# Kernel tuning notes

Measured on AMD Instinct MI355X. Metric: run time of the kernel, lower is better.

## Reference

```python
import jax, jax.numpy as jnp
import numpy as np

N_NODES = 50000
D_FEAT = 128
N_EDGES = 500000


def setup_inputs() -> dict:
    key = jax.random.key(0)
    ks = jax.random.split(key, 9)
    scale1 = 1.0 / np.sqrt(2 * D_FEAT)
    scale2 = 1.0 / np.sqrt(512)
    scale3 = 1.0 / np.sqrt(256)
    return {
        "node_features": jax.random.normal(ks[0], (N_NODES, D_FEAT), dtype=jnp.float32),
        "edge_label_index": jax.random.randint(ks[1], (2, N_EDGES), 0, N_NODES, dtype=jnp.int64),
        "W1": jax.random.normal(ks[2], (512, 2 * D_FEAT), dtype=jnp.float32) * scale1,
        "b1": jax.random.normal(ks[3], (512,), dtype=jnp.float32) * scale1,
        "W2": jax.random.normal(ks[4], (256, 512), dtype=jnp.float32) * scale2,
        "b2": jax.random.normal(ks[5], (256,), dtype=jnp.float32) * scale2,
        "W3": jax.random.normal(ks[6], (1, 256), dtype=jnp.float32) * scale3,
        "b3": jax.random.normal(ks[7], (1,), dtype=jnp.float32) * scale3,
    }


def reference(node_features, edge_label_index, W1, b1, W2, b2, W3, b3):
    row = edge_label_index[0]
    col = edge_label_index[1]
    # [E, 2*d] gather + concat
    x = jnp.concatenate([node_features[row], node_features[col]], axis=-1)
    x = jax.nn.relu(x @ W1.T + b1)          # [E, 512]
    x = jax.nn.relu(x @ W2.T + b2)          # [E, 256]
    intermediate_x = x
    logits = x @ W3.T + b3                  # [E, 1]
    return (logits.reshape(-1), intermediate_x)
```

## Files before the change

kernel.cpp:

```cpp
#include <hip/hip_runtime.h>
#include <stdint.h>

#define E_TOT 500000
#define EB 64
#define NBLK ((E_TOT + EB - 1) / EB)
#define SWZ(e) (((e) & 7) << 4)
#define HOFF 32768

using u32x4  = __attribute__((ext_vector_type(4))) unsigned int;
using f32x4  = __attribute__((ext_vector_type(4))) float;
using short8 = __attribute__((ext_vector_type(8))) short;

__device__ __forceinline__ uint32_t f2bf(float x) {
    uint32_t u = __builtin_bit_cast(uint32_t, x);
    return (u + 0x7fffu + ((u >> 16) & 1u)) >> 16;
}
__device__ __forceinline__ uint32_t pk2(float a, float b) {
    return f2bf(a) | (f2bf(b) << 16);
}

__global__ void prep_weights(const float* __restrict__ W1, const float* __restrict__ W2,
                             unsigned short* __restrict__ w1b, unsigned short* __restrict__ w2b) {
    int t = blockIdx.x * 256 + threadIdx.x;
    int i = t * 4;
    if (i < 131072) {
        float4 f = *reinterpret_cast<const float4*>(W1 + i);
        uint2 u;
        u.x = pk2(f.x, f.y); u.y = pk2(f.z, f.w);
        *reinterpret_cast<uint2*>(w1b + i) = u;
    } else {
        int j = i - 131072;
        float4 f = *reinterpret_cast<const float4*>(W2 + j);
        uint2 u;
        u.x = pk2(f.x, f.y); u.y = pk2(f.z, f.w);
        *reinterpret_cast<uint2*>(w2b + j) = u;
    }
}

#define CHUNK(ABASE, MTSTR, LDSOFF, ACC, CUR, NXT, C, LAST)                                  \
  {                                                                                          \
    if (!(LAST)) {                                                                           \
      _Pragma("unroll") for (int kkl = 0; kkl < 2; ++kkl)                                    \
        _Pragma("unroll") for (int mt = 0; mt < 4; ++mt)                                     \
          NXT[kkl][mt] = *reinterpret_cast<const short8*>(                                   \
              (ABASE) + mt * (MTSTR) + (((C) + 1) * 2 + kkl) * 64);                          \
    }                                                                                        \
    _Pragma("unroll") for (int kkl = 0; kkl < 2; ++kkl) {                                    \
      const int kk = (C) * 2 + kkl;                                                          \
      short8 bfr[4];                                                                         \
      _Pragma("unroll") for (int nt = 0; nt < 4; ++nt) {                                     \
        const int boff = ((kk & 1) ? (bx0[nt] ^ 64) : bx0[nt]) + (LDSOFF) + (kk >> 1) * 128; \
        bfr[nt] = *reinterpret_cast<const short8*>(smem + boff);                             \
      }                                                                                      \
      _Pragma("unroll") for (int nt = 0; nt < 4; ++nt)                                       \
        _Pragma("unroll") for (int mt = 0; mt < 4; ++mt)                                     \
          ACC[mt][nt] = __builtin_amdgcn_mfma_f32_16x16x32_bf16(                             \
              CUR[kkl][mt], bfr[nt], ACC[mt][nt], 0, 0, 0);                                  \
    }                                                                                        \
  }

#define PHASE(ABASE, MTSTR, LDSOFF, ACC)                                                     \
  {                                                                                          \
    _Pragma("unroll") for (int kkl = 0; kkl < 2; ++kkl)                                      \
      _Pragma("unroll") for (int mt = 0; mt < 4; ++mt)                                       \
        Aa[kkl][mt] = *reinterpret_cast<const short8*>((ABASE) + mt * (MTSTR) + kkl * 64);   \
    CHUNK(ABASE, MTSTR, LDSOFF, ACC, Aa, Ab, 0, 0)                                           \
    CHUNK(ABASE, MTSTR, LDSOFF, ACC, Ab, Aa, 1, 0)                                           \
    CHUNK(ABASE, MTSTR, LDSOFF, ACC, Aa, Ab, 2, 0)                                           \
    CHUNK(ABASE, MTSTR, LDSOFF, ACC, Ab, Aa, 3, 1)                                           \
  }

template<bool PREPPED>
__global__ __launch_bounds__(256, 2) void fused_mlp(
    const float* __restrict__ nf,
    const int* __restrict__ eidx,
    const char* __restrict__ w1p,
    const char* __restrict__ w2p,
    const float* __restrict__ b1,
    const float* __restrict__ b2,
    const float* __restrict__ w3,
    const float* __restrict__ b3,
    float* __restrict__ out)
{
    __shared__ __align__(16) char smem[65536];
    __shared__ float logit_part[4][EB];

    const int tid  = threadIdx.x;
    const int lane = tid & 63;
    const int wid  = tid >> 6;
    const int hi   = lane >> 4;
    const int lo   = lane & 15;
    const long long e0 = (long long)blockIdx.x * EB;

    {
        int e    = tid >> 2;
        int side = (tid >> 1) & 1;
        int half = tid & 1;
        long long eg = e0 + e;
        int idx = 0;
        if (eg < E_TOT) idx = eidx[(size_t)side * E_TOT + (size_t)eg];
        const float4* src = reinterpret_cast<const float4*>(nf + (size_t)idx * 128 + half * 64);
        char* dstrow = smem + e * 512;
        const int ob = side * 256 + half * 128;
#pragma unroll
        for (int c = 0; c < 8; ++c) {
            float4 f0 = src[2 * c];
            float4 f1 = src[2 * c + 1];
            u32x4 u;
            u[0] = pk2(f0.x, f0.y); u[1] = pk2(f0.z, f0.w);
            u[2] = pk2(f1.x, f1.y); u[3] = pk2(f1.z, f1.w);
            *reinterpret_cast<u32x4*>(dstrow + ((ob + c * 16) ^ SWZ(e))) = u;
        }
    }

    int bx0[4];
#pragma unroll
    for (int nt = 0; nt < 4; ++nt) {
        int e   = nt * 16 + lo;
        int low = (hi * 16) ^ ((e & 3) << 4);
        int s6  = (e >> 2) & 1;
        bx0[nt] = e * 512 + low + 64 * s6;
    }

    __syncthreads();

    f32x4 acc2[4][4];
#pragma unroll
    for (int mt = 0; mt < 4; ++mt)
#pragma unroll
        for (int nt = 0; nt < 4; ++nt)
            acc2[mt][nt] = f32x4{0.f, 0.f, 0.f, 0.f};

    short8 Aa[2][4], Ab[2][4];

#pragma unroll
    for (int h = 0; h < 2; ++h) {
        f32x4 acc1[4][4];
#pragma unroll
        for (int mt = 0; mt < 4; ++mt)
#pragma unroll
            for (int nt = 0; nt < 4; ++nt)
                acc1[mt][nt] = f32x4{0.f, 0.f, 0.f, 0.f};

        if constexpr (PREPPED) {
            const char* a1b = w1p + (size_t)(h * 256 + wid * 64 + lo) * 512 + hi * 16;
            PHASE(a1b, (16 * 512), 0, acc1)
        } else {
            const float* W1f = reinterpret_cast<const float*>(w1p);
#pragma unroll
            for (int kk = 0; kk < 8; ++kk) {
                short8 a[4], b[4];
#pragma unroll
                for (int mt = 0; mt < 4; ++mt) {
                    const int row = h * 256 + wid * 64 + mt * 16 + lo;
                    const float* p = W1f + (size_t)row * 256 + kk * 32 + hi * 8;
                    float4 f0 = *reinterpret_cast<const float4*>(p);
                    float4 f1 = *reinterpret_cast<const float4*>(p + 4);
                    u32x4 u;
                    u[0] = pk2(f0.x, f0.y); u[1] = pk2(f0.z, f0.w);
                    u[2] = pk2(f1.x, f1.y); u[3] = pk2(f1.z, f1.w);
                    a[mt] = __builtin_bit_cast(short8, u);
                }
#pragma unroll
                for (int nt = 0; nt < 4; ++nt) {
                    const int boff = ((kk & 1) ? (bx0[nt] ^ 64) : bx0[nt]) + (kk >> 1) * 128;
                    b[nt] = *reinterpret_cast<const short8*>(smem + boff);
                }
#pragma unroll
                for (int nt = 0; nt < 4; ++nt)
#pragma unroll
                    for (int mt = 0; mt < 4; ++mt)
                        acc1[mt][nt] = __builtin_amdgcn_mfma_f32_16x16x32_bf16(a[mt], b[nt], acc1[mt][nt], 0, 0, 0);
            }
        }

#pragma unroll
        for (int mt = 0; mt < 4; ++mt) {
            const float4 bias = *reinterpret_cast<const float4*>(b1 + h * 256 + wid * 64 + mt * 16 + hi * 4);
            const int ob = wid * 128 + mt * 32 + hi * 8;
#pragma unroll
            for (int nt = 0; nt < 4; ++nt) {
                int e = nt * 16 + lo;
                f32x4 v = acc1[mt][nt];
                float r0 = fmaxf(v[0] + bias.x, 0.f);
                float r1 = fmaxf(v[1] + bias.y, 0.f);
                float r2 = fmaxf(v[2] + bias.z, 0.f);
                float r3 = fmaxf(v[3] + bias.w, 0.f);
                uint2 u;
                u.x = pk2(r0, r1); u.y = pk2(r2, r3);
                *reinterpret_cast<uint2*>(smem + HOFF + e * 512 + (ob ^ SWZ(e))) = u;
            }
        }
        __syncthreads();

        if constexpr (PREPPED) {
            const char* a2b = w2p + (size_t)(wid * 64 + lo) * 1024 + h * 512 + hi * 16;
            PHASE(a2b, (16 * 1024), HOFF, acc2)
        } else {
            const float* W2f = reinterpret_cast<const float*>(w2p);
#pragma unroll
            for (int kk = 0; kk < 8; ++kk) {
                short8 a[4], b[4];
#pragma unroll
                for (int mt = 0; mt < 4; ++mt) {
                    const int row = wid * 64 + mt * 16 + lo;
                    const float* p = W2f + (size_t)row * 512 + h * 256 + kk * 32 + hi * 8;
                    float4 f0 = *reinterpret_cast<const float4*>(p);
                    float4 f1 = *reinterpret_cast<const float4*>(p + 4);
                    u32x4 u;
                    u[0] = pk2(f0.x, f0.y); u[1] = pk2(f0.z, f0.w);
                    u[2] = pk2(f1.x, f1.y); u[3] = pk2(f1.z, f1.w);
                    a[mt] = __builtin_bit_cast(short8, u);
                }
#pragma unroll
                for (int nt = 0; nt < 4; ++nt) {
                    const int boff = ((kk & 1) ? (bx0[nt] ^ 64) : bx0[nt]) + HOFF + (kk >> 1) * 128;
                    b[nt] = *reinterpret_cast<const short8*>(smem + boff);
                }
#pragma unroll
                for (int nt = 0; nt < 4; ++nt)
#pragma unroll
                    for (int mt = 0; mt < 4; ++mt)
                        acc2[mt][nt] = __builtin_amdgcn_mfma_f32_16x16x32_bf16(a[mt], b[nt], acc2[mt][nt], 0, 0, 0);
            }
        }
        if (h == 0) __syncthreads();
    }

    {
        float* inter = out + E_TOT;
        float pls[4] = {0.f, 0.f, 0.f, 0.f};
#pragma unroll
        for (int mt = 0; mt < 4; ++mt) {
            const int m = wid * 64 + mt * 16 + hi * 4;
            const float4 bias = *reinterpret_cast<const float4*>(b2 + m);
            const float4 wv   = *reinterpret_cast<const float4*>(w3 + m);
#pragma unroll
            for (int nt = 0; nt < 4; ++nt) {
                long long eg = e0 + nt * 16 + lo;
                f32x4 v = acc2[mt][nt];
                float4 hh;
                hh.x = fmaxf(v[0] + bias.x, 0.f);
                hh.y = fmaxf(v[1] + bias.y, 0.f);
                hh.z = fmaxf(v[2] + bias.z, 0.f);
                hh.w = fmaxf(v[3] + bias.w, 0.f);
                if (eg < E_TOT)
                    *reinterpret_cast<float4*>(inter + (size_t)eg * 256 + m) = hh;
                pls[nt] += hh.x * wv.x + hh.y * wv.y + hh.z * wv.z + hh.w * wv.w;
            }
        }
#pragma unroll
        for (int nt = 0; nt < 4; ++nt) {
            float p = pls[nt];
            p += __shfl_xor(p, 16);
            p += __shfl_xor(p, 32);
            if (hi == 0) logit_part[wid][nt * 16 + lo] = p;
        }
    }
    __syncthreads();
    if (tid < EB) {
        long long eg = e0 + tid;
        if (eg < E_TOT) {
            float s = b3[0];
#pragma unroll
            for (int w = 0; w < 4; ++w) s += logit_part[w][tid];
            out[eg] = s;
        }
    }
}

extern "C" void kernel_launch(void* const* d_in, const int* in_sizes, int n_in,
                              void* d_out, int out_size, void* d_ws, size_t ws_size,
                              hipStream_t stream) {
    const float* nf   = (const float*)d_in[0];
    const int*   eidx = (const int*)d_in[1];
    const float* W1   = (const float*)d_in[2];
    const float* b1   = (const float*)d_in[3];
    const float* W2   = (const float*)d_in[4];
    const float* b2   = (const float*)d_in[5];
    const float* W3   = (const float*)d_in[6];
    const float* b3   = (const float*)d_in[7];
    float* out = (float*)d_out;

    const size_t need = (size_t)(512 * 256 + 256 * 512) * 2;
    if (ws_size >= need) {
        unsigned short* w1b = (unsigned short*)d_ws;
        unsigned short* w2b = w1b + 512 * 256;
        prep_weights<<<256, 256, 0, stream>>>(W1, W2, w1b, w2b);
        fused_mlp<true><<<NBLK, 256, 0, stream>>>(nf, eidx, (const char*)w1b, (const char*)w2b,
                                                  b1, b2, W3, b3, out);
    } else {
        fused_mlp<false><<<NBLK, 256, 0, stream>>>(nf, eidx, (const char*)W1, (const char*)W2,
                                                   b1, b2, W3, b3, out);
    }
}
```

Measured before the change: 587.4 us.

## Split layer-1 GEMM into half-width chunks and double-buffer A/B fragment loads

Layer 1 is now computed in two 32-row chunks per wave, so only 8 accumulator tiles are live instead of 16. This lowers register pressure next to the persistent layer-2 accumulators. The phase macro is rewritten to double-buffer both the global weight fragments and the LDS activation fragments one k-step ahead, where before only weights were prefetched two k-steps ahead. The cost is that each layer-1 chunk re-reads the LDS B fragments, doubling those reads, and the prefetch distance for global loads is shorter.

```diff
diff --git a/kernel.cpp b/kernel.cpp
--- a/kernel.cpp
+++ b/kernel.cpp
@@ -37,37 +37,31 @@
     }
 }
 
-#define CHUNK(ABASE, MTSTR, LDSOFF, ACC, CUR, NXT, C, LAST)                                  \
+#define PHASEPP(ABASE, MTSTR, NMT, LDSOFF, ACC)                                              \
   {                                                                                          \
-    if (!(LAST)) {                                                                           \
-      _Pragma("unroll") for (int kkl = 0; kkl < 2; ++kkl)                                    \
-        _Pragma("unroll") for (int mt = 0; mt < 4; ++mt)                                     \
-          NXT[kkl][mt] = *reinterpret_cast<const short8*>(                                   \
-              (ABASE) + mt * (MTSTR) + (((C) + 1) * 2 + kkl) * 64);                          \
-    }                                                                                        \
-    _Pragma("unroll") for (int kkl = 0; kkl < 2; ++kkl) {                                    \
-      const int kk = (C) * 2 + kkl;                                                          \
-      short8 bfr[4];                                                                         \
-      _Pragma("unroll") for (int nt = 0; nt < 4; ++nt) {                                     \
-        const int boff = ((kk & 1) ? (bx0[nt] ^ 64) : bx0[nt]) + (LDSOFF) + (kk >> 1) * 128; \
-        bfr[nt] = *reinterpret_cast<const short8*>(smem + boff);                             \
+    short8 Af[2][4];                                                                         \
+    short8 Bf[2][4];                                                                         \
+    _Pragma("unroll") for (int mt = 0; mt < (NMT); ++mt)                                     \
+      Af[0][mt] = *reinterpret_cast<const short8*>((ABASE) + mt * (MTSTR));                  \
+    _Pragma("unroll") for (int nt = 0; nt < 4; ++nt)                                         \
+      Bf[0][nt] = *reinterpret_cast<const short8*>(smem + bx0[nt] + (LDSOFF));               \
+    _Pragma("unroll") for (int kk = 0; kk < 8; ++kk) {                                       \
+      const int cur = kk & 1, nxt = cur ^ 1;                                                 \
+      if (kk < 7) {                                                                          \
+        _Pragma("unroll") for (int mt = 0; mt < (NMT); ++mt)                                 \
+          Af[nxt][mt] = *reinterpret_cast<const short8*>(                                    \
+              (ABASE) + mt * (MTSTR) + (kk + 1) * 64);                                       \
+        _Pragma("unroll") for (int nt = 0; nt < 4; ++nt) {                                   \
+          const int boff = (((kk + 1) & 1) ? (bx0[nt] ^ 64) : bx0[nt])                       \
+                           + (LDSOFF) + ((kk + 1) >> 1) * 128;                               \
+          Bf[nxt][nt] = *reinterpret_cast<const short8*>(smem + boff);                       \
+        }                                                                                    \
       }                                                                                      \
       _Pragma("unroll") for (int nt = 0; nt < 4; ++nt)                                       \
-        _Pragma("unroll") for (int mt = 0; mt < 4; ++mt)                                     \
+        _Pragma("unroll") for (int mt = 0; mt < (NMT); ++mt)                                 \
           ACC[mt][nt] = __builtin_amdgcn_mfma_f32_16x16x32_bf16(                             \
-              CUR[kkl][mt], bfr[nt], ACC[mt][nt], 0, 0, 0);                                  \
+              Af[cur][mt], Bf[cur][nt], ACC[mt][nt], 0, 0, 0);                               \
     }                                                                                        \
-  }
-
-#define PHASE(ABASE, MTSTR, LDSOFF, ACC)                                                     \
-  {                                                                                          \
-    _Pragma("unroll") for (int kkl = 0; kkl < 2; ++kkl)                                      \
-      _Pragma("unroll") for (int mt = 0; mt < 4; ++mt)                                       \
-        Aa[kkl][mt] = *reinterpret_cast<const short8*>((ABASE) + mt * (MTSTR) + kkl * 64);   \
-    CHUNK(ABASE, MTSTR, LDSOFF, ACC, Aa, Ab, 0, 0)                                           \
-    CHUNK(ABASE, MTSTR, LDSOFF, ACC, Ab, Aa, 1, 0)                                           \
-    CHUNK(ABASE, MTSTR, LDSOFF, ACC, Aa, Ab, 2, 0)                                           \
-    CHUNK(ABASE, MTSTR, LDSOFF, ACC, Ab, Aa, 3, 1)                                           \
   }
 
 template<bool PREPPED>
@@ -131,71 +125,73 @@
         for (int nt = 0; nt < 4; ++nt)
             acc2[mt][nt] = f32x4{0.f, 0.f, 0.f, 0.f};
 
-    short8 Aa[2][4], Ab[2][4];
-
 #pragma unroll
     for (int h = 0; h < 2; ++h) {
-        f32x4 acc1[4][4];
-#pragma unroll
-        for (int mt = 0; mt < 4; ++mt)
-#pragma unroll
-            for (int nt = 0; nt < 4; ++nt)
-                acc1[mt][nt] = f32x4{0.f, 0.f, 0.f, 0.f};
-
-        if constexpr (PREPPED) {
-            const char* a1b = w1p + (size_t)(h * 256 + wid * 64 + lo) * 512 + hi * 16;
-            PHASE(a1b, (16 * 512), 0, acc1)
-        } else {
-            const float* W1f = reinterpret_cast<const float*>(w1p);
-#pragma unroll
-            for (int kk = 0; kk < 8; ++kk) {
-                short8 a[4], b[4];
-#pragma unroll
-                for (int mt = 0; mt < 4; ++mt) {
-                    const int row = h * 256 + wid * 64 + mt * 16 + lo;
-                    const float* p = W1f + (size_t)row * 256 + kk * 32 + hi * 8;
-                    float4 f0 = *reinterpret_cast<const float4*>(p);
-                    float4 f1 = *reinterpret_cast<const float4*>(p + 4);
-                    u32x4 u;
-                    u[0] = pk2(f0.x, f0.y); u[1] = pk2(f0.z, f0.w);
-                    u[2] = pk2(f1.x, f1.y); u[3] = pk2(f1.z, f1.w);
-                    a[mt] = __builtin_bit_cast(short8, u);
-                }
+#pragma unroll
+        for (int c = 0; c < 2; ++c) {
+            f32x4 acc1[2][4];
+#pragma unroll
+            for (int mt = 0; mt < 2; ++mt)
+#pragma unroll
+                for (int nt = 0; nt < 4; ++nt)
+                    acc1[mt][nt] = f32x4{0.f, 0.f, 0.f, 0.f};
+
+            if constexpr (PREPPED) {
+                const char* a1b = w1p + (size_t)(h * 256 + wid * 64 + c * 32 + lo) * 512 + hi * 16;
+                PHASEPP(a1b, (16 * 512), 2, 0, acc1)
+            } else {
+                const float* W1f = reinterpret_cast<const float*>(w1p);
+#pragma unroll
+                for (int kk = 0; kk < 8; ++kk) {
+                    short8 a[2], b[4];
+#pragma unroll
+                    for (int mt = 0; mt < 2; ++mt) {
+                        const int row = h * 256 + wid * 64 + c * 32 + mt * 16 + lo;
+                        const float* p = W1f + (size_t)row * 256 + kk * 32 + hi * 8;
+                        float4 f0 = *reinterpret_cast<const float4*>(p);
+                        float4 f1 = *reinterpret_cast<const float4*>(p + 4);
+                        u32x4 u;
+                        u[0] = pk2(f0.x, f0.y); u[1] = pk2(f0.z, f0.w);
+                        u[2] = pk2(f1.x, f1.y); u[3] = pk2(f1.z, f1.w);
+                        a[mt] = __builtin_bit_cast(short8, u);
+                    }
+#pragma unroll
+                    for (int nt = 0; nt < 4; ++nt) {
+                        const int boff = ((kk & 1) ? (bx0[nt] ^ 64) : bx0[nt]) + (kk >> 1) * 128;
+                        b[nt] = *reinterpret_cast<const short8*>(smem + boff);
+                    }
+#pragma unroll
+                    for (int nt = 0; nt < 4; ++nt)
+#pragma unroll
+                        for (int mt = 0; mt < 2; ++mt)
+                            acc1[mt][nt] = __builtin_amdgcn_mfma_f32_16x16x32_bf16(a[mt], b[nt], acc1[mt][nt], 0, 0, 0);
+                }
+            }
+
+#pragma unroll
+            for (int mt = 0; mt < 2; ++mt) {
+                const float4 bias = *reinterpret_cast<const float4*>(
+                    b1 + h * 256 + wid * 64 + c * 32 + mt * 16 + hi * 4);
+                const int ob = wid * 128 + c * 64 + mt * 32 + hi * 8;
 #pragma unroll
                 for (int nt = 0; nt < 4; ++nt) {
-                    const int boff = ((kk & 1) ? (bx0[nt] ^ 64) : bx0[nt]) + (kk >> 1) * 128;
-                    b[nt] = *reinterpret_cast<const short8*>(smem + boff);
-                }
-#pragma unroll
-                for (int nt = 0; nt < 4; ++nt)
-#pragma unroll
-                    for (int mt = 0; mt < 4; ++mt)
-                        acc1[mt][nt] = __builtin_amdgcn_mfma_f32_16x16x32_bf16(a[mt], b[nt], acc1[mt][nt], 0, 0, 0);
-            }
-        }
-
-#pragma unroll
-        for (int mt = 0; mt < 4; ++mt) {
-            const float4 bias = *reinterpret_cast<const float4*>(b1 + h * 256 + wid * 64 + mt * 16 + hi * 4);
-            const int ob = wid * 128 + mt * 32 + hi * 8;
-#pragma unroll
-            for (int nt = 0; nt < 4; ++nt) {
-                int e = nt * 16 + lo;
-                f32x4 v = acc1[mt][nt];
-                float r0 = fmaxf(v[0] + bias.x, 0.f);
-                float r1 = fmaxf(v[1] + bias.y, 0.f);
-                float r2 = fmaxf(v[2] + bias.z, 0.f);
-                float r3 = fmaxf(v[3] + bias.w, 0.f);
-                uint2 u;
-                u.x = pk2(r0, r1); u.y = pk2(r2, r3);
-                *reinterpret_cast<uint2*>(smem + HOFF + e * 512 + (ob ^ SWZ(e))) = u;
+                    int e = nt * 16 + lo;
+                    f32x4 v = acc1[mt][nt];
+                    float r0 = fmaxf(v[0] + bias.x, 0.f);
+                    float r1 = fmaxf(v[1] + bias.y, 0.f);
+                    float r2 = fmaxf(v[2] + bias.z, 0.f);
+                    float r3 = fmaxf(v[3] + bias.w, 0.f);
+                    uint2 u;
+                    u.x = pk2(r0, r1); u.y = pk2(r2, r3);
+                    *reinterpret_cast<uint2*>(smem + HOFF + e * 512 + (ob ^ SWZ(e))) = u;
+                }
             }
         }
         __syncthreads();
 
         if constexpr (PREPPED) {
             const char* a2b = w2p + (size_t)(wid * 64 + lo) * 1024 + h * 512 + hi * 16;
-            PHASE(a2b, (16 * 1024), HOFF, acc2)
+            PHASEPP(a2b, (16 * 1024), 4, HOFF, acc2)
         } else {
             const float* W2f = reinterpret_cast<const float*>(w2p);
 #pragma unroll
```

New measurement: 637.5 us. +8.5%, slower.
